# Optimization experiments

Measured on AMD Instinct MI355X. Metric: run time of the kernel, lower is better.

Reference implementation:

```python
import jax, jax.numpy as jnp
import numpy as np

LOSS_WEIGHT = 1.0
BIG = 1e9  # finite sentinel for masked-out pixels (avoids inf-grad NaNs)


def setup_inputs() -> dict:
    key = jax.random.key(0)
    k1, k2 = jax.random.split(key)
    B, N, H, W = 4, 6890, 64, 64
    vert2d = jax.random.uniform(k1, (B, N, 2), dtype=jnp.float32) * jnp.array([W, H], jnp.float32)
    mask = jax.random.randint(k2, (B, H, W), 0, 2, dtype=jnp.int32)
    return {"vert2d": vert2d, "mask": mask}


def reference(vert2d, mask):
    B, N, _ = vert2d.shape
    _, H, W = mask.shape
    scale = jnp.array([W, H], vert2d.dtype)
    v = vert2d / scale  # [B,N,2], normalized
    # all pixel coords as (x, y), normalized -- the dense equivalent of torch.where points
    ys, xs = jnp.meshgrid(jnp.arange(H), jnp.arange(W), indexing="ij")
    pts = (jnp.stack([xs.ravel(), ys.ravel()], axis=-1).astype(v.dtype) / scale)  # [HW,2]
    valid = (mask.reshape(B, -1) > 0)  # [B,HW] boolean membership of each pixel
    # pairwise L2 distances: [B,N,HW]
    diff = v[:, :, None, :] - pts[None, None, :, :]
    d = jnp.sqrt(jnp.sum(diff * diff, axis=-1))
    dm = jnp.where(valid[:, None, :], d, BIG)
    # sum over mask points of min over verts  +  sum over verts of min over mask points
    loss = jnp.sum(jnp.min(dm, axis=1) * valid) + jnp.sum(jnp.min(dm, axis=2))
    return LOSS_WEIGHT * loss
```

## Files before the change

kernel.cpp:

```cpp
#include <hip/hip_runtime.h>

#define NB 4
#define NV 6890
#define HW 4096
#define NPAD 6912
#define C1 32
#define T1CS 216
#define C2 16
#define T1_BLOCKS 512
#define T2_BLOCKS 448
#define NRED_BLOCKS 172

#define OFF_T1P 0
#define OFF_T2P 2097152
#define OFF_SUM 3866624
#define OFF_TKT 3866628

#define FINF 3.402823466e38f
#define PBIG 1.0e18f

__global__ __launch_bounds__(256) void k_main(const float* __restrict__ vert,
                                              const int* __restrict__ mask,
                                              float* __restrict__ t1p,
                                              float* __restrict__ t2p,
                                              float* __restrict__ sum,
                                              unsigned* __restrict__ tkt) {
    __shared__ float4 lds[256];
    int bx = blockIdx.x, tid = threadIdx.x;
    if (bx == 0 && tid == 0) { *sum = 0.f; *tkt = 0u; }
    if (bx < T1_BLOCKS) {
        int c = bx & 31, q = (bx >> 5) & 3, b = bx >> 7;
        if (tid < T1CS) {
            int n = c * T1CS + tid;
            float4 w = make_float4(0.f, 0.f, PBIG, 0.f);
            if (n < NV) {
                float2 v = reinterpret_cast<const float2*>(vert)[b * NV + n];
                w = make_float4(-2.f * v.x, -2.f * v.y, fmaf(v.x, v.x, v.y * v.y), 0.f);
            }
            lds[tid] = w;
        }
        __syncthreads();
        int x = tid & 63, ry = tid >> 6;
        float fx  = (float)x;
        float fy0 = (float)(q * 16 + ry);
        float fy1 = fy0 + 4.f, fy2 = fy0 + 8.f, fy3 = fy0 + 12.f;
        float m0 = FINF, m1 = FINF, m2 = FINF, m3 = FINF;
        #pragma unroll 4
        for (int i = 0; i < T1CS; i += 2) {
            float4 a = lds[i], g2 = lds[i + 1];
            float ta = fmaf(a.x,  fx, a.z);
            float tg = fmaf(g2.x, fx, g2.z);
            m0 = fminf(m0, fminf(fmaf(a.y, fy0, ta), fmaf(g2.y, fy0, tg)));
            m1 = fminf(m1, fminf(fmaf(a.y, fy1, ta), fmaf(g2.y, fy1, tg)));
            m2 = fminf(m2, fminf(fmaf(a.y, fy2, ta), fmaf(g2.y, fy2, tg)));
            m3 = fminf(m3, fminf(fmaf(a.y, fy3, ta), fmaf(g2.y, fy3, tg)));
        }
        float fx2 = fx * fx;
        int y0 = q * 16 + ry;
        float* tp = t1p + ((c * NB + b) << 12) + x;
        tp[(y0     ) * 64] = fmaf(fy0, fy0, fx2) + m0;
        tp[(y0 +  4) * 64] = fmaf(fy1, fy1, fx2) + m1;
        tp[(y0 +  8) * 64] = fmaf(fy2, fy2, fx2) + m2;
        tp[(y0 + 12) * 64] = fmaf(fy3, fy3, fx2) + m3;
    } else {
        int t2i = bx - T1_BLOCKS;
        int pc = t2i & 15;
        int r  = t2i >> 4;
        int g  = r % 7, b = r / 7;
        {
            int pix = pc * 256 + tid;
            float fx = (float)(pix & 63), fy = (float)(pix >> 6);
            float pz = (mask[b * HW + pix] > 0) ? fmaf(fx, fx, fy * fy) : PBIG;
            lds[tid] = make_float4(-2.f * fx, -2.f * fy, pz, 0.f);
        }
        __syncthreads();
        int n0 = g * 1024 + tid;
        const float2* vv = reinterpret_cast<const float2*>(vert) + b * NV;
        float vx[4], vy[4];
        bool  val[4];
        #pragma unroll
        for (int k = 0; k < 4; ++k) {
            int n = n0 + 256 * k;
            val[k] = (n < NV);
            float2 t = val[k] ? vv[n] : make_float2(0.f, 0.f);
            vx[k] = t.x; vy[k] = t.y;
        }
        float mm[4] = {FINF, FINF, FINF, FINF};
        #pragma unroll 2
        for (int j = 0; j < 256; j += 2) {
            float4 a = lds[j], cc = lds[j + 1];
            #pragma unroll
            for (int k = 0; k < 4; ++k) {
                float da = fmaf(a.x,  vx[k], fmaf(a.y,  vy[k], a.z));
                float dc = fmaf(cc.x, vx[k], fmaf(cc.y, vy[k], cc.z));
                mm[k] = fminf(mm[k], fminf(da, dc));
            }
        }
        float* op = t2p + pc * (NB * NPAD) + b * NPAD + n0;
        #pragma unroll
        for (int k = 0; k < 4; ++k)
            if (val[k]) op[256 * k] = mm[k] + fmaf(vx[k], vx[k], vy[k] * vy[k]);
    }
}

__global__ __launch_bounds__(256) void k_red(const float* __restrict__ t1p,
                                             const float* __restrict__ t2p,
                                             const int* __restrict__ mask,
                                             float* __restrict__ sum,
                                             unsigned* __restrict__ tkt,
                                             float* __restrict__ out) {
    int gid = blockIdx.x * 256 + threadIdx.x;
    float v = 0.f;
    if (gid < NB * HW) {
        if (mask[gid] > 0) {
            float m = FINF;
            #pragma unroll
            for (int c = 0; c < C1; ++c) m = fminf(m, t1p[c * (NB * HW) + gid]);
            v = sqrtf(fmaxf(m, 0.f)) * (1.0f / 64.0f);
        }
    } else {
        int j = gid - NB * HW;
        int b = j / NPAD;
        int n = j - b * NPAD;
        if (n < NV) {
            float m = FINF;
            #pragma unroll
            for (int pc = 0; pc < C2; ++pc) m = fminf(m, t2p[pc * (NB * NPAD) + j]);
            v = sqrtf(fmaxf(m, 0.f)) * (1.0f / 64.0f);
        }
    }
    __shared__ float sbuf[4];
    __shared__ bool last;
    for (int off = 32; off; off >>= 1) v += __shfl_down(v, off, 64);
    int lane = threadIdx.x & 63, wid = threadIdx.x >> 6;
    if (!lane) sbuf[wid] = v;
    __syncthreads();
    if (threadIdx.x == 0) {
        float bs = sbuf[0] + sbuf[1] + sbuf[2] + sbuf[3];
        atomicAdd(sum, bs);
        __threadfence();
        unsigned t = atomicAdd(tkt, 1u);
        last = (t == NRED_BLOCKS - 1);
    }
    __syncthreads();
    if (last && threadIdx.x == 0)
        out[0] = atomicAdd(sum, 0.f);
}

extern "C" void kernel_launch(void* const* d_in, const int* in_sizes, int n_in,
                              void* d_out, int out_size, void* d_ws, size_t ws_size,
                              hipStream_t stream) {
    const float* vert = (const float*)d_in[0];
    const int*   mask = (const int*)d_in[1];
    char* ws = (char*)d_ws;
    float*    t1p = (float*)(ws + OFF_T1P);
    float*    t2p = (float*)(ws + OFF_T2P);
    float*    sum = (float*)(ws + OFF_SUM);
    unsigned* tkt = (unsigned*)(ws + OFF_TKT);
    float*    out = (float*)d_out;

    k_main<<<T1_BLOCKS + T2_BLOCKS, 256, 0, stream>>>(vert, mask, t1p, t2p, sum, tkt);
    k_red <<<NRED_BLOCKS, 256, 0, stream>>>(t1p, t2p, mask, sum, tkt, out);
}
```

Baseline: 79.92 us.

## Enlarge per-thread tiles and factor row term out of vertex-to-pixel inner loop

Pass 1 now computes 8 rows per thread, which halves the block count and reuses each LDS vertex load across more pixels. Pass 2 splits each pixel chunk into two rows and hoists the y-dependent term out of the inner loop, so each vertex-pixel pair costs one FMA plus a min. Each thread also handles 16 vertices and the chunk count doubles to 32, so the t2 partial buffer grows and the reduction reads twice as many partials. Register pressure rises and the grid shrinks to 512 blocks, which may reduce occupancy.

```diff
diff --git a/kernel.cpp b/kernel.cpp
--- a/kernel.cpp
+++ b/kernel.cpp
@@ -6,15 +6,15 @@
 #define NPAD 6912
 #define C1 32
 #define T1CS 216
-#define C2 16
-#define T1_BLOCKS 512
-#define T2_BLOCKS 448
+#define C2 32
+#define T1_BLOCKS 256
+#define T2_BLOCKS 256
 #define NRED_BLOCKS 172
 
 #define OFF_T1P 0
 #define OFF_T2P 2097152
-#define OFF_SUM 3866624
-#define OFF_TKT 3866628
+#define OFF_SUM 6291456
+#define OFF_TKT 6291460
 
 #define FINF 3.402823466e38f
 #define PBIG 1.0e18f
@@ -25,11 +25,12 @@
                                               float* __restrict__ t2p,
                                               float* __restrict__ sum,
                                               unsigned* __restrict__ tkt) {
-    __shared__ float4 lds[256];
+    __shared__ float4 lds4[T1CS];
+    float2* lds2 = reinterpret_cast<float2*>(lds4);
     int bx = blockIdx.x, tid = threadIdx.x;
     if (bx == 0 && tid == 0) { *sum = 0.f; *tkt = 0u; }
     if (bx < T1_BLOCKS) {
-        int c = bx & 31, q = (bx >> 5) & 3, b = bx >> 7;
+        int c = bx & 31, q = (bx >> 5) & 1, b = bx >> 6;
         if (tid < T1CS) {
             int n = c * T1CS + tid;
             float4 w = make_float4(0.f, 0.f, PBIG, 0.f);
@@ -37,69 +38,81 @@
                 float2 v = reinterpret_cast<const float2*>(vert)[b * NV + n];
                 w = make_float4(-2.f * v.x, -2.f * v.y, fmaf(v.x, v.x, v.y * v.y), 0.f);
             }
-            lds[tid] = w;
+            lds4[tid] = w;
         }
         __syncthreads();
         int x = tid & 63, ry = tid >> 6;
-        float fx  = (float)x;
-        float fy0 = (float)(q * 16 + ry);
-        float fy1 = fy0 + 4.f, fy2 = fy0 + 8.f, fy3 = fy0 + 12.f;
-        float m0 = FINF, m1 = FINF, m2 = FINF, m3 = FINF;
+        float fx = (float)x;
+        float fy[8], m[8];
+        #pragma unroll
+        for (int k = 0; k < 8; ++k) { fy[k] = (float)(q * 32 + ry + 4 * k); m[k] = FINF; }
         #pragma unroll 4
         for (int i = 0; i < T1CS; i += 2) {
-            float4 a = lds[i], g2 = lds[i + 1];
+            float4 a = lds4[i], g2 = lds4[i + 1];
             float ta = fmaf(a.x,  fx, a.z);
             float tg = fmaf(g2.x, fx, g2.z);
-            m0 = fminf(m0, fminf(fmaf(a.y, fy0, ta), fmaf(g2.y, fy0, tg)));
-            m1 = fminf(m1, fminf(fmaf(a.y, fy1, ta), fmaf(g2.y, fy1, tg)));
-            m2 = fminf(m2, fminf(fmaf(a.y, fy2, ta), fmaf(g2.y, fy2, tg)));
-            m3 = fminf(m3, fminf(fmaf(a.y, fy3, ta), fmaf(g2.y, fy3, tg)));
+            #pragma unroll
+            for (int k = 0; k < 8; ++k)
+                m[k] = fminf(m[k], fminf(fmaf(a.y, fy[k], ta), fmaf(g2.y, fy[k], tg)));
         }
         float fx2 = fx * fx;
-        int y0 = q * 16 + ry;
         float* tp = t1p + ((c * NB + b) << 12) + x;
-        tp[(y0     ) * 64] = fmaf(fy0, fy0, fx2) + m0;
-        tp[(y0 +  4) * 64] = fmaf(fy1, fy1, fx2) + m1;
-        tp[(y0 +  8) * 64] = fmaf(fy2, fy2, fx2) + m2;
-        tp[(y0 + 12) * 64] = fmaf(fy3, fy3, fx2) + m3;
+        #pragma unroll
+        for (int k = 0; k < 8; ++k) {
+            int y = q * 32 + ry + 4 * k;
+            tp[y * 64] = fmaf(fy[k], fy[k], fx2) + m[k];
+        }
     } else {
         int t2i = bx - T1_BLOCKS;
-        int pc = t2i & 15;
-        int r  = t2i >> 4;
-        int g  = r % 7, b = r / 7;
-        {
-            int pix = pc * 256 + tid;
-            float fx = (float)(pix & 63), fy = (float)(pix >> 6);
-            float pz = (mask[b * HW + pix] > 0) ? fmaf(fx, fx, fy * fy) : PBIG;
-            lds[tid] = make_float4(-2.f * fx, -2.f * fy, pz, 0.f);
+        int pc = t2i & 31, g = (t2i >> 5) & 1, b = t2i >> 6;
+        if (tid < 128) {
+            int r = tid >> 6, j = tid & 63;
+            int pix = (pc * 2 + r) * 64 + j;
+            float fx = (float)j;
+            float e = (mask[b * HW + pix] > 0) ? fx * fx : PBIG;
+            lds2[tid] = make_float2(-2.f * fx, e);
         }
         __syncthreads();
-        int n0 = g * 1024 + tid;
-        const float2* vv = reinterpret_cast<const float2*>(vert) + b * NV;
-        float vx[4], vy[4];
-        bool  val[4];
+        int n0 = g * 4096 + tid;
+        const float2* vv2 = reinterpret_cast<const float2*>(vert) + b * NV;
+        float vx[16], vy[16], vv[16], acc[16];
+        bool val[16];
         #pragma unroll
-        for (int k = 0; k < 4; ++k) {
+        for (int k = 0; k < 16; ++k) {
             int n = n0 + 256 * k;
             val[k] = (n < NV);
-            float2 t = val[k] ? vv[n] : make_float2(0.f, 0.f);
+            float2 t = val[k] ? vv2[n] : make_float2(0.f, 0.f);
             vx[k] = t.x; vy[k] = t.y;
+            vv[k] = fmaf(t.x, t.x, t.y * t.y);
         }
-        float mm[4] = {FINF, FINF, FINF, FINF};
-        #pragma unroll 2
-        for (int j = 0; j < 256; j += 2) {
-            float4 a = lds[j], cc = lds[j + 1];
+        #pragma unroll
+        for (int r = 0; r < 2; ++r) {
+            float fyr  = (float)(pc * 2 + r);
+            float fm2y = -2.f * fyr;
+            float mr[16];
             #pragma unroll
-            for (int k = 0; k < 4; ++k) {
-                float da = fmaf(a.x,  vx[k], fmaf(a.y,  vy[k], a.z));
-                float dc = fmaf(cc.x, vx[k], fmaf(cc.y, vy[k], cc.z));
-                mm[k] = fminf(mm[k], fminf(da, dc));
+            for (int k = 0; k < 16; ++k) mr[k] = FINF;
+            #pragma unroll 2
+            for (int j = 0; j < 64; j += 2) {
+                float2 a = lds2[r * 64 + j], cc = lds2[r * 64 + j + 1];
+                #pragma unroll
+                for (int k = 0; k < 16; ++k) {
+                    float da = fmaf(a.x,  vx[k], a.y);
+                    float dc = fmaf(cc.x, vx[k], cc.y);
+                    mr[k] = fminf(mr[k], fminf(da, dc));
+                }
+            }
+            #pragma unroll
+            for (int k = 0; k < 16; ++k) {
+                float base = fmaf(fm2y, vy[k], fmaf(fyr, fyr, vv[k]));
+                float rv = mr[k] + base;
+                acc[k] = r ? fminf(acc[k], rv) : rv;
             }
         }
-        float* op = t2p + pc * (NB * NPAD) + b * NPAD + n0;
+        float* op = t2p + pc * (NB * 8192) + b * 8192 + n0;
         #pragma unroll
-        for (int k = 0; k < 4; ++k)
-            if (val[k]) op[256 * k] = mm[k] + fmaf(vx[k], vx[k], vy[k] * vy[k]);
+        for (int k = 0; k < 16; ++k)
+            if (val[k]) op[256 * k] = acc[k];
     }
 }
 
@@ -114,7 +127,7 @@
     if (gid < NB * HW) {
         if (mask[gid] > 0) {
             float m = FINF;
-            #pragma unroll
+            #pragma unroll 8
             for (int c = 0; c < C1; ++c) m = fminf(m, t1p[c * (NB * HW) + gid]);
             v = sqrtf(fmaxf(m, 0.f)) * (1.0f / 64.0f);
         }
@@ -124,8 +137,8 @@
         int n = j - b * NPAD;
         if (n < NV) {
             float m = FINF;
-            #pragma unroll
-            for (int pc = 0; pc < C2; ++pc) m = fminf(m, t2p[pc * (NB * NPAD) + j]);
+            #pragma unroll 8
+            for (int pc = 0; pc < C2; ++pc) m = fminf(m, t2p[pc * (NB * 8192) + b * 8192 + n]);
             v = sqrtf(fmaxf(m, 0.f)) * (1.0f / 64.0f);
         }
     }
```

Result: faster. 78.33 us (-2.0%).
